# Optimization experiments

Measured on AMD Instinct MI355X. Metric: run time of the kernel, lower is better.

The kernel has to match this reference:

```python
import jax, jax.numpy as jnp
import numpy as np

N_NODES = 100000
N_EDGES = 1600000


def _cheb_norm(edge_index, num_nodes):
    # PyG ChebConv norm with sym normalization, lambda_max=2:
    # remove self-loops, L = I - D^-1/2 A D^-1/2, scale by 2/lambda_max (=1),
    # add self-loops with -1 -> diagonal nets to 0, leaving w = -d^-1/2 d^-1/2 on edges.
    src, dst = edge_index[0], edge_index[1]
    mask = (src != dst).astype(jnp.float32)  # remove_self_loops
    deg = jax.ops.segment_sum(mask, src, num_segments=num_nodes)
    dinv = jnp.where(deg > 0, jax.lax.rsqrt(jnp.maximum(deg, 1.0)), 0.0)
    w = -dinv[src] * dinv[dst] * mask
    return w


def _cheb_conv(x, src, dst, w_edge, W, b, num_nodes):
    # W: [K=3, C_in, C_out], Chebyshev recurrence T0=x, T1=Lx, T2=2L T1 - T0
    def prop(h):
        return jax.ops.segment_sum(w_edge[:, None] * h[src], dst, num_segments=num_nodes)

    tx0 = x
    tx1 = prop(x)
    tx2 = 2.0 * prop(tx1) - tx0
    out = tx0 @ W[0] + tx1 @ W[1] + tx2 @ W[2] + b
    return out


def setup_inputs() -> dict:
    key = jax.random.key(0)
    ks = jax.random.split(key, 10)
    x = jax.random.normal(ks[0], (N_NODES, 128), dtype=jnp.float32)
    edge_index = jax.random.randint(ks[1], (2, N_EDGES), 0, N_NODES, dtype=jnp.int64)
    batch = jnp.zeros((N_NODES,), dtype=jnp.int64)

    def glorot(k, shape):
        fan = shape[-2] + shape[-1]
        return jax.random.uniform(k, shape, jnp.float32, -1.0, 1.0) * np.sqrt(6.0 / fan)

    W1 = glorot(ks[2], (3, 128, 64))
    b1 = jnp.zeros((64,), jnp.float32)
    W2 = glorot(ks[3], (3, 64, 128))
    b2 = jnp.zeros((128,), jnp.float32)
    W3 = glorot(ks[4], (3, 128, 256))
    b3 = jnp.zeros((256,), jnp.float32)
    return {"x": x, "edge_index": edge_index, "batch": batch,
            "W1": W1, "b1": b1, "W2": W2, "b2": b2, "W3": W3, "b3": b3}


def reference(x, edge_index, batch, W1, b1, W2, b2, W3, b3):
    num_nodes = x.shape[0]
    src, dst = edge_index[0], edge_index[1]
    w_edge = _cheb_norm(edge_index, num_nodes)
    h = jax.nn.relu(_cheb_conv(x, src, dst, w_edge, W1, b1, num_nodes))
    h = jax.nn.relu(_cheb_conv(h, src, dst, w_edge, W2, b2, num_nodes))
    h = _cheb_conv(h, src, dst, w_edge, W3, b3, num_nodes)
    return h
```

## Files before the change

kernel.cpp:

```cpp
#include <hip/hip_runtime.h>

#define N_NODES 100000
#define N_EDGES 1600000
#define CAP 64
#define GB 6250
#define GM 782

typedef short short8 __attribute__((ext_vector_type(8)));
typedef float f32x4 __attribute__((ext_vector_type(4)));

__device__ __forceinline__ unsigned short f2b(float f) {
    unsigned u = __builtin_bit_cast(unsigned, f);
    u += 0x7fffu + ((u >> 16) & 1u);
    return (unsigned short)(u >> 16);
}
__device__ __forceinline__ float b2f_lo(unsigned p) {
    return __builtin_bit_cast(float, p << 16);
}
__device__ __forceinline__ float b2f_hi(unsigned p) {
    return __builtin_bit_cast(float, p & 0xffff0000u);
}

__global__ __launch_bounds__(256) void k_fat(const int* __restrict__ src, const int* __restrict__ dst,
                                             float* __restrict__ degout, int* __restrict__ cnt,
                                             int* __restrict__ slots,
                                             const float* __restrict__ x, const float* __restrict__ W1,
                                             const float* __restrict__ b1,
                                             const float* __restrict__ W2, const float* __restrict__ W3,
                                             unsigned short* __restrict__ vub,
                                             unsigned short* __restrict__ Wt2,
                                             unsigned short* __restrict__ Wt3) {
    constexpr int KT = 128, KP = KT + 8, NFR = 4;
    __shared__ unsigned short sw[64 * KP];
    const int tid = threadIdx.x;
    int bid = blockIdx.x;

    if (bid < GB) {
        int e = bid * 256 + tid;
        int s = src[e], d = dst[e];
        if (s != d) {
            atomicAdd(&degout[s], 1.0f);
            int pos = atomicAdd(&cnt[d], 1);
            if (pos < CAP) slots[(size_t)d * CAP + pos] = s;
        }
        return;
    }
    bid -= GB;
    if (bid < 3 * GM) {
        const int sl = bid / GM, mb = bid % GM;
        const int n0 = sl * 64;

        for (int i = tid; i < 64 * 128; i += 256) {
            int k = i >> 6;
            int r = i & 63;
            int co = r + n0;
            float v;
            if (co < 64)       v = W1[(128 + k) * 64 + co];
            else if (co < 128) v = W1[(256 + k) * 64 + (co - 64)];
            else               v = W1[k * 64 + (co - 128)] - W1[(256 + k) * 64 + (co - 128)];
            sw[r * KP + k] = f2b(v);
        }
        __syncthreads();

        const int wave = tid >> 6, lane = tid & 63;
        const int l16 = lane & 15, quad = lane >> 4;
        const int mBase = mb * 128 + wave * 32;
        const int r0 = mBase + l16, r1 = mBase + 16 + l16;
        const bool in0 = r0 < N_NODES, in1 = r1 < N_NODES;

        f32x4 acc[2][NFR] = {};
        const short8 zero8 = {0, 0, 0, 0, 0, 0, 0, 0};

        #pragma unroll
        for (int kt = 0; kt < KT / 32; kt++) {
            const int kin = kt * 32 + quad * 8;
            short8 a0 = zero8, a1 = zero8;
            if (in0) {
                const float* px = x + (size_t)r0 * 128 + kin;
                float4 f0 = *(const float4*)px, f1 = *(const float4*)(px + 4);
                a0[0] = (short)f2b(f0.x); a0[1] = (short)f2b(f0.y);
                a0[2] = (short)f2b(f0.z); a0[3] = (short)f2b(f0.w);
                a0[4] = (short)f2b(f1.x); a0[5] = (short)f2b(f1.y);
                a0[6] = (short)f2b(f1.z); a0[7] = (short)f2b(f1.w);
            }
            if (in1) {
                const float* px = x + (size_t)r1 * 128 + kin;
                float4 f0 = *(const float4*)px, f1 = *(const float4*)(px + 4);
                a1[0] = (short)f2b(f0.x); a1[1] = (short)f2b(f0.y);
                a1[2] = (short)f2b(f0.z); a1[3] = (short)f2b(f0.w);
                a1[4] = (short)f2b(f1.x); a1[5] = (short)f2b(f1.y);
                a1[6] = (short)f2b(f1.z); a1[7] = (short)f2b(f1.w);
            }
            #pragma unroll
            for (int nf = 0; nf < NFR; nf++) {
                const short8 b = *(const short8*)(sw + (nf * 16 + l16) * KP + kt * 32 + quad * 8);
                acc[0][nf] = __builtin_amdgcn_mfma_f32_16x16x32_bf16(a0, b, acc[0][nf], 0, 0, 0);
                acc[1][nf] = __builtin_amdgcn_mfma_f32_16x16x32_bf16(a1, b, acc[1][nf], 0, 0, 0);
            }
        }

        #pragma unroll
        for (int mi = 0; mi < 2; mi++) {
            #pragma unroll
            for (int nf = 0; nf < NFR; nf++) {
                #pragma unroll
                for (int r = 0; r < 4; r++) {
                    const int node = mBase + mi * 16 + quad * 4 + r;
                    if (node < N_NODES) {
                        const int co = n0 + nf * 16 + l16;
                        float o = acc[mi][nf][r] + (co >= 128 ? b1[co - 128] : 0.f);
                        vub[(size_t)node * 192 + co] = f2b(o);
                    }
                }
            }
        }
        return;
    }
    bid -= 3 * GM;
    if (bid < 96) {
        int j = bid * 256 + tid;
        int k = j % 192, n = j / 192;
        Wt2[(size_t)n * 192 + k] = f2b(W2[(size_t)k * 128 + n]);
        return;
    }
    bid -= 96;
    {
        int j = bid * 256 + tid;
        int k = j % 384, n = j / 384;
        Wt3[(size_t)n * 384 + k] = f2b(W3[(size_t)k * 256 + n]);
    }
}

__global__ void k_dinv(float* __restrict__ deg) {
    int n = blockIdx.x * blockDim.x + threadIdx.x;
    if (n < N_NODES) {
        float dg = deg[n];
        deg[n] = dg > 0.f ? rsqrtf(dg) : 0.f;
    }
}

template <int C, bool RELU>
__global__ __launch_bounds__(256) void k_gather7(const unsigned short* __restrict__ h,
                                                 int hStride,
                                                 const int* __restrict__ cnt,
                                                 const int* __restrict__ slots,
                                                 const float* __restrict__ dinv,
                                                 float alpha,
                                                 const unsigned short* __restrict__ init,
                                                 int iStride,
                                                 float beta,
                                                 unsigned short* __restrict__ out) {
    const int wave = threadIdx.x >> 6;
    const int lane = threadIdx.x & 63;
    const int half = lane >> 5;
    const int l32  = lane & 31;
    const int n0 = (blockIdx.x * 4 + wave) * 2;
    if (n0 >= N_NODES) return;
    const int n1 = n0 + 1;
    const int m0 = min(cnt[n0], CAP);
    const int m1 = min(cnt[n1], CAP);
    const int nMy = half ? n1 : n0;

    int c0l = 0, c1l = 0;
    float w0f = 0.f, w1f = 0.f;
    if (lane < m0) { c0l = slots[(size_t)n0 * CAP + lane]; w0f = dinv[c0l]; }
    if (lane < m1) { c1l = slots[(size_t)n1 * CAP + lane]; w1f = dinv[c1l]; }
    const int w0i = __builtin_bit_cast(int, w0f);
    const int w1i = __builtin_bit_cast(int, w1f);

    const int mhi = max(m0, m1);
    const float scale = -alpha * dinv[nMy];

    if (C == 128) {
        const uint2* h4 = (const uint2*)h;
        float ax = 0.f, ay = 0.f, az = 0.f, aw = 0.f;
        for (int j = 0; j < mhi; j += 8) {
            #pragma unroll
            for (int k = 0; k < 8; k++) {
                int cA = __builtin_amdgcn_readlane(c0l, j + k);
                int cB = __builtin_amdgcn_readlane(c1l, j + k);
                float wA = __builtin_bit_cast(float, __builtin_amdgcn_readlane(w0i, j + k));
                float wB = __builtin_bit_cast(float, __builtin_amdgcn_readlane(w1i, j + k));
                int c = half ? cB : cA;
                float w = half ? wB : wA;
                uint2 q = h4[(size_t)c * hStride + l32];
                ax = fmaf(w, b2f_lo(q.x), ax); ay = fmaf(w, b2f_hi(q.x), ay);
                az = fmaf(w, b2f_lo(q.y), az); aw = fmaf(w, b2f_hi(q.y), aw);
            }
        }
        float vx = scale * ax, vy = scale * ay, vz = scale * az, vw = scale * aw;
        if (init) {
            uint2 ip = ((const uint2*)init)[(size_t)nMy * iStride + l32];
            vx = fmaf(beta, b2f_lo(ip.x), vx); vy = fmaf(beta, b2f_hi(ip.x), vy);
            vz = fmaf(beta, b2f_lo(ip.y), vz); vw = fmaf(beta, b2f_hi(ip.y), vw);
        }
        if (RELU) {
            vx = fmaxf(vx, 0.f); vy = fmaxf(vy, 0.f);
            vz = fmaxf(vz, 0.f); vw = fmaxf(vw, 0.f);
        }
        uint2 o;
        o.x = (unsigned)f2b(vx) | ((unsigned)f2b(vy) << 16);
        o.y = (unsigned)f2b(vz) | ((unsigned)f2b(vw) << 16);
        ((uint2*)out)[(size_t)nMy * 32 + l32] = o;
    } else {
        const unsigned* h2 = (const unsigned*)h;
        float ax = 0.f, ay = 0.f;
        for (int j = 0; j < mhi; j += 8) {
            #pragma unroll
            for (int k = 0; k < 8; k++) {
                int cA = __builtin_amdgcn_readlane(c0l, j + k);
                int cB = __builtin_amdgcn_readlane(c1l, j + k);
                float wA = __builtin_bit_cast(float, __builtin_amdgcn_readlane(w0i, j + k));
                float wB = __builtin_bit_cast(float, __builtin_amdgcn_readlane(w1i, j + k));
                int c = half ? cB : cA;
                float w = half ? wB : wA;
                unsigned q = h2[(size_t)c * hStride + l32];
                ax = fmaf(w, b2f_lo(q), ax); ay = fmaf(w, b2f_hi(q), ay);
            }
        }
        float vx = scale * ax, vy = scale * ay;
        if (init) {
            unsigned ip = ((const unsigned*)init)[(size_t)nMy * iStride + l32];
            vx = fmaf(beta, b2f_lo(ip), vx); vy = fmaf(beta, b2f_hi(ip), vy);
        }
        if (RELU) { vx = fmaxf(vx, 0.f); vy = fmaxf(vy, 0.f); }
        ((unsigned*)out)[(size_t)nMy * 32 + l32] =
            (unsigned)f2b(vx) | ((unsigned)f2b(vy) << 16);
    }
}

template <int CIN, int COUT, int NSL, bool RELU, bool BF16OUT>
__global__ __launch_bounds__(256) void k_mm2(const unsigned short* __restrict__ t0,
                                             const unsigned short* __restrict__ t1,
                                             const unsigned short* __restrict__ t2,
                                             const unsigned short* __restrict__ Wt,
                                             const float* __restrict__ bias,
                                             void* __restrict__ outv) {
    constexpr int KT = 3 * CIN;
    constexpr int KP = KT + 8;
    constexpr int NFR = NSL / 16;
    __shared__ unsigned short sw[NSL * KP];

    const int tid = threadIdx.x;
    const int n0 = blockIdx.y * NSL;

    constexpr int CHUNKS = NSL * KT / 8;
    for (int i = tid; i < CHUNKS; i += 256) {
        int row = i / (KT / 8);
        int k8 = i % (KT / 8);
        short8 v = *(const short8*)(Wt + (size_t)(n0 + row) * KT + k8 * 8);
        *(short8*)(sw + row * KP + k8 * 8) = v;
    }
    __syncthreads();

    const int wave = tid >> 6, lane = tid & 63;
    const int l16 = lane & 15, quad = lane >> 4;
    const int mBase = blockIdx.x * 128 + wave * 32;
    const int r0 = mBase + l16, r1 = mBase + 16 + l16;
    const bool in0 = r0 < N_NODES, in1 = r1 < N_NODES;

    f32x4 acc[2][NFR] = {};
    const unsigned short* tb[3] = {t0, t1, t2};
    const short8 zero8 = {0, 0, 0, 0, 0, 0, 0, 0};

    #pragma unroll
    for (int kt = 0; kt < KT / 32; kt++) {
        const int kb = kt * 32;
        const unsigned short* t = tb[kb / CIN];
        const int kin = (kb % CIN) + quad * 8;
        short8 a0 = zero8, a1 = zero8;
        if (in0) a0 = *(const short8*)(t + (size_t)r0 * CIN + kin);
        if (in1) a1 = *(const short8*)(t + (size_t)r1 * CIN + kin);
        #pragma unroll
        for (int nf = 0; nf < NFR; nf++) {
            const short8 b = *(const short8*)(sw + (nf * 16 + l16) * KP + kb + quad * 8);
            acc[0][nf] = __builtin_amdgcn_mfma_f32_16x16x32_bf16(a0, b, acc[0][nf], 0, 0, 0);
            acc[1][nf] = __builtin_amdgcn_mfma_f32_16x16x32_bf16(a1, b, acc[1][nf], 0, 0, 0);
        }
    }

    #pragma unroll
    for (int mi = 0; mi < 2; mi++) {
        #pragma unroll
        for (int nf = 0; nf < NFR; nf++) {
            #pragma unroll
            for (int r = 0; r < 4; r++) {
                const int node = mBase + mi * 16 + quad * 4 + r;
                if (node < N_NODES) {
                    const int co = n0 + nf * 16 + l16;
                    float o = acc[mi][nf][r] + bias[co];
                    if (RELU) o = fmaxf(o, 0.f);
                    if (BF16OUT)
                        ((unsigned short*)outv)[(size_t)node * COUT + co] = f2b(o);
                    else
                        ((float*)outv)[(size_t)node * COUT + co] = o;
                }
            }
        }
    }
}

template <int CIN, int COUT, int NSL>
__global__ __launch_bounds__(256) void k_mm3(const unsigned short* __restrict__ t0,
                                             const unsigned short* __restrict__ t1,
                                             const unsigned short* __restrict__ t2,
                                             const unsigned short* __restrict__ Wt,
                                             const float* __restrict__ bias,
                                             float* __restrict__ out) {
    constexpr int KT = 3 * CIN;
    constexpr int KP = KT + 8;
    constexpr int NFR = NSL / 16;
    constexpr int NSLICES = COUT / NSL;
    constexpr int KSTEPS = KT / 32;
    __shared__ unsigned short sw[NSL * KP];

    const int tid = threadIdx.x;
    const int wave = tid >> 6, lane = tid & 63;
    const int l16 = lane & 15, quad = lane >> 4;
    const int mBase = blockIdx.x * 128 + wave * 32;
    const int r0 = mBase + l16, r1 = mBase + 16 + l16;
    const bool in0 = r0 < N_NODES, in1 = r1 < N_NODES;

    const unsigned short* tb[3] = {t0, t1, t2};
    const short8 zero8 = {0, 0, 0, 0, 0, 0, 0, 0};

    short8 a0[KSTEPS], a1[KSTEPS];
    #pragma unroll
    for (int kt = 0; kt < KSTEPS; kt++) {
        const int kb = kt * 32;
        const unsigned short* t = tb[kb / CIN];
        const int kin = (kb % CIN) + quad * 8;
        a0[kt] = in0 ? *(const short8*)(t + (size_t)r0 * CIN + kin) : zero8;
        a1[kt] = in1 ? *(const short8*)(t + (size_t)r1 * CIN + kin) : zero8;
    }

    constexpr int CHUNKS = NSL * KT / 8;
    for (int ns = 0; ns < NSLICES; ns++) {
        const int n0 = ns * NSL;
        if (ns) __syncthreads();
        for (int i = tid; i < CHUNKS; i += 256) {
            int row = i / (KT / 8);
            int k8 = i % (KT / 8);
            *(short8*)(sw + row * KP + k8 * 8) =
                *(const short8*)(Wt + (size_t)(n0 + row) * KT + k8 * 8);
        }
        __syncthreads();

        f32x4 acc[2][NFR] = {};
        #pragma unroll
        for (int kt = 0; kt < KSTEPS; kt++) {
            #pragma unroll
            for (int nf = 0; nf < NFR; nf++) {
                const short8 b = *(const short8*)(sw + (nf * 16 + l16) * KP + kt * 32 + quad * 8);
                acc[0][nf] = __builtin_amdgcn_mfma_f32_16x16x32_bf16(a0[kt], b, acc[0][nf], 0, 0, 0);
                acc[1][nf] = __builtin_amdgcn_mfma_f32_16x16x32_bf16(a1[kt], b, acc[1][nf], 0, 0, 0);
            }
        }

        #pragma unroll
        for (int mi = 0; mi < 2; mi++) {
            #pragma unroll
            for (int nf = 0; nf < NFR; nf++) {
                #pragma unroll
                for (int r = 0; r < 4; r++) {
                    const int node = mBase + mi * 16 + quad * 4 + r;
                    if (node < N_NODES) {
                        const int co = n0 + nf * 16 + l16;
                        out[(size_t)node * COUT + co] = acc[mi][nf][r] + bias[co];
                    }
                }
            }
        }
    }
}

static inline int ceil_div(int a, int b) { return (a + b - 1) / b; }

extern "C" void kernel_launch(void* const* d_in, const int* in_sizes, int n_in,
                              void* d_out, int out_size, void* d_ws, size_t ws_size,
                              hipStream_t stream) {
    const float* x   = (const float*)d_in[0];
    const int*   ei  = (const int*)d_in[1];
    const int*   src = ei;
    const int*   dst = ei + N_EDGES;
    const float* W1 = (const float*)d_in[3];
    const float* b1 = (const float*)d_in[4];
    const float* W2 = (const float*)d_in[5];
    const float* b2 = (const float*)d_in[6];
    const float* W3 = (const float*)d_in[7];
    const float* b3 = (const float*)d_in[8];
    float* out = (float*)d_out;

    char* p = (char*)d_ws;
    int*   slots  = (int*)p;             p += (size_t)N_NODES * CAP * 4;
    float* dinv   = (float*)p;           p += (size_t)N_NODES * 4;
    int*   cnt    = (int*)p;             p += (size_t)N_NODES * 4;
    unsigned short* tx1b = (unsigned short*)p; p += (size_t)N_NODES * 128 * 2;
    unsigned short* h1b  = (unsigned short*)p; p += (size_t)N_NODES * 64 * 2;
    unsigned short* tx2b = (unsigned short*)p; p += (size_t)N_NODES * 128 * 2;
    unsigned short* h2b  = (unsigned short*)p; p += (size_t)N_NODES * 128 * 2;
    unsigned short* Wt2  = (unsigned short*)p; p += (size_t)128 * 192 * 2;
    unsigned short* Wt3  = (unsigned short*)p; p += (size_t)256 * 384 * 2;
    unsigned short* vub = tx2b;

    const int TB = 256;
    const int gN = ceil_div(N_NODES, TB);
    const int gG = ceil_div(N_NODES, 8);
    const int gM = ceil_div(N_NODES, 128);
    const int FATB = GB + 3 * GM + 96 + 384;

    hipMemsetAsync(dinv, 0, 2 * N_NODES * sizeof(float), stream);
    k_fat<<<FATB, TB, 0, stream>>>(src, dst, dinv, cnt, slots,
                                   x, W1, b1, W2, W3, vub, Wt2, Wt3);
    k_dinv<<<gN, TB, 0, stream>>>(dinv);

    k_gather7<64, false><<<gG, TB, 0, stream>>>(vub + 64, 96, cnt, slots, dinv,
                                                2.f, vub, 96, 1.f, tx1b);
    k_gather7<64, true><<<gG, TB, 0, stream>>>(tx1b, 32, cnt, slots, dinv,
                                               1.f, vub + 128, 96, 1.f, h1b);

    k_gather7<64, false><<<gG, TB, 0, stream>>>(h1b, 32, cnt, slots, dinv,
                                                1.f, nullptr, 0, 0.f, tx1b);
    k_gather7<64, false><<<gG, TB, 0, stream>>>(tx1b, 32, cnt, slots, dinv,
                                                2.f, h1b, 32, -1.f, tx2b);
    k_mm2<64, 128, 128, true, true><<<dim3(gM, 1), TB, 0, stream>>>(h1b, tx1b, tx2b, Wt2, b2, h2b);

    k_gather7<128, false><<<gG, TB, 0, stream>>>(h2b, 32, cnt, slots, dinv,
                                                 1.f, nullptr, 0, 0.f, tx1b);
    k_gather7<128, false><<<gG, TB, 0, stream>>>(tx1b, 32, cnt, slots, dinv,
                                                 2.f, h2b, 32, -1.f, tx2b);
    k_mm3<128, 256, 64><<<dim3(gM, 1), TB, 0, stream>>>(h2b, tx1b, tx2b, Wt3, b3, out);
}
```

Baseline: 770.6 us.

## Reuse loaded x rows across three weight slices and interleave fat-kernel blocks

Each GEMM block in the fused first kernel now loads and converts its 128 rows of x to bf16 once, keeps them in registers, and loops over the three 64-column weight slices itself. Before, three separate blocks each reloaded the same rows. The block index is also permuted with a multiplicative swizzle (7919 mod grid size) so edge-scatter, GEMM and transpose blocks are interleaved across the GPU. This cuts redundant x reads and balances atomic-heavy and MFMA-heavy work. In exchange there are fewer, longer GEMM blocks, extra syncs, more register pressure, and the swizzle is only a bijection if 7919 is coprime with the grid size.

```diff
diff --git a/kernel.cpp b/kernel.cpp
--- a/kernel.cpp
+++ b/kernel.cpp
@@ -5,6 +5,8 @@
 #define CAP 64
 #define GB 6250
 #define GM 782
+#define FATB (GB + GM + 96 + 384)
+#define SWZ 7919
 
 typedef short short8 __attribute__((ext_vector_type(8)));
 typedef float f32x4 __attribute__((ext_vector_type(4)));
@@ -33,7 +35,7 @@
     constexpr int KT = 128, KP = KT + 8, NFR = 4;
     __shared__ unsigned short sw[64 * KP];
     const int tid = threadIdx.x;
-    int bid = blockIdx.x;
+    int bid = (int)(((unsigned)blockIdx.x * SWZ) % FATB);
 
     if (bid < GB) {
         int e = bid * 256 + tid;
@@ -46,77 +48,83 @@
         return;
     }
     bid -= GB;
-    if (bid < 3 * GM) {
-        const int sl = bid / GM, mb = bid % GM;
-        const int n0 = sl * 64;
-
-        for (int i = tid; i < 64 * 128; i += 256) {
-            int k = i >> 6;
-            int r = i & 63;
-            int co = r + n0;
-            float v;
-            if (co < 64)       v = W1[(128 + k) * 64 + co];
-            else if (co < 128) v = W1[(256 + k) * 64 + (co - 64)];
-            else               v = W1[k * 64 + (co - 128)] - W1[(256 + k) * 64 + (co - 128)];
-            sw[r * KP + k] = f2b(v);
-        }
-        __syncthreads();
-
+    if (bid < GM) {
         const int wave = tid >> 6, lane = tid & 63;
         const int l16 = lane & 15, quad = lane >> 4;
-        const int mBase = mb * 128 + wave * 32;
+        const int mBase = bid * 128 + wave * 32;
         const int r0 = mBase + l16, r1 = mBase + 16 + l16;
         const bool in0 = r0 < N_NODES, in1 = r1 < N_NODES;
-
-        f32x4 acc[2][NFR] = {};
         const short8 zero8 = {0, 0, 0, 0, 0, 0, 0, 0};
 
+        short8 a0[4], a1[4];
         #pragma unroll
-        for (int kt = 0; kt < KT / 32; kt++) {
+        for (int kt = 0; kt < 4; kt++) {
             const int kin = kt * 32 + quad * 8;
-            short8 a0 = zero8, a1 = zero8;
+            short8 t0 = zero8, t1 = zero8;
             if (in0) {
                 const float* px = x + (size_t)r0 * 128 + kin;
                 float4 f0 = *(const float4*)px, f1 = *(const float4*)(px + 4);
-                a0[0] = (short)f2b(f0.x); a0[1] = (short)f2b(f0.y);
-                a0[2] = (short)f2b(f0.z); a0[3] = (short)f2b(f0.w);
-                a0[4] = (short)f2b(f1.x); a0[5] = (short)f2b(f1.y);
-                a0[6] = (short)f2b(f1.z); a0[7] = (short)f2b(f1.w);
+                t0[0] = (short)f2b(f0.x); t0[1] = (short)f2b(f0.y);
+                t0[2] = (short)f2b(f0.z); t0[3] = (short)f2b(f0.w);
+                t0[4] = (short)f2b(f1.x); t0[5] = (short)f2b(f1.y);
+                t0[6] = (short)f2b(f1.z); t0[7] = (short)f2b(f1.w);
             }
             if (in1) {
                 const float* px = x + (size_t)r1 * 128 + kin;
                 float4 f0 = *(const float4*)px, f1 = *(const float4*)(px + 4);
-                a1[0] = (short)f2b(f0.x); a1[1] = (short)f2b(f0.y);
-                a1[2] = (short)f2b(f0.z); a1[3] = (short)f2b(f0.w);
-                a1[4] = (short)f2b(f1.x); a1[5] = (short)f2b(f1.y);
-                a1[6] = (short)f2b(f1.z); a1[7] = (short)f2b(f1.w);
-            }
-            #pragma unroll
-            for (int nf = 0; nf < NFR; nf++) {
-                const short8 b = *(const short8*)(sw + (nf * 16 + l16) * KP + kt * 32 + quad * 8);
-                acc[0][nf] = __builtin_amdgcn_mfma_f32_16x16x32_bf16(a0, b, acc[0][nf], 0, 0, 0);
-                acc[1][nf] = __builtin_amdgcn_mfma_f32_16x16x32_bf16(a1, b, acc[1][nf], 0, 0, 0);
-            }
-        }
-
-        #pragma unroll
-        for (int mi = 0; mi < 2; mi++) {
-            #pragma unroll
-            for (int nf = 0; nf < NFR; nf++) {
+                t1[0] = (short)f2b(f0.x); t1[1] = (short)f2b(f0.y);
+                t1[2] = (short)f2b(f0.z); t1[3] = (short)f2b(f0.w);
+                t1[4] = (short)f2b(f1.x); t1[5] = (short)f2b(f1.y);
+                t1[6] = (short)f2b(f1.z); t1[7] = (short)f2b(f1.w);
+            }
+            a0[kt] = t0; a1[kt] = t1;
+        }
+
+        for (int sl = 0; sl < 3; sl++) {
+            const int n0 = sl * 64;
+            if (sl) __syncthreads();
+            for (int i = tid; i < 64 * 128; i += 256) {
+                int k = i >> 6;
+                int r = i & 63;
+                int co = r + n0;
+                float v;
+                if (co < 64)       v = W1[(128 + k) * 64 + co];
+                else if (co < 128) v = W1[(256 + k) * 64 + (co - 64)];
+                else               v = W1[k * 64 + (co - 128)] - W1[(256 + k) * 64 + (co - 128)];
+                sw[r * KP + k] = f2b(v);
+            }
+            __syncthreads();
+
+            f32x4 acc[2][NFR] = {};
+            #pragma unroll
+            for (int kt = 0; kt < 4; kt++) {
                 #pragma unroll
-                for (int r = 0; r < 4; r++) {
-                    const int node = mBase + mi * 16 + quad * 4 + r;
-                    if (node < N_NODES) {
-                        const int co = n0 + nf * 16 + l16;
-                        float o = acc[mi][nf][r] + (co >= 128 ? b1[co - 128] : 0.f);
-                        vub[(size_t)node * 192 + co] = f2b(o);
+                for (int nf = 0; nf < NFR; nf++) {
+                    const short8 b = *(const short8*)(sw + (nf * 16 + l16) * KP + kt * 32 + quad * 8);
+                    acc[0][nf] = __builtin_amdgcn_mfma_f32_16x16x32_bf16(a0[kt], b, acc[0][nf], 0, 0, 0);
+                    acc[1][nf] = __builtin_amdgcn_mfma_f32_16x16x32_bf16(a1[kt], b, acc[1][nf], 0, 0, 0);
+                }
+            }
+
+            #pragma unroll
+            for (int mi = 0; mi < 2; mi++) {
+                #pragma unroll
+                for (int nf = 0; nf < NFR; nf++) {
+                    #pragma unroll
+                    for (int r = 0; r < 4; r++) {
+                        const int node = mBase + mi * 16 + quad * 4 + r;
+                        if (node < N_NODES) {
+                            const int co = n0 + nf * 16 + l16;
+                            float o = acc[mi][nf][r] + (co >= 128 ? b1[co - 128] : 0.f);
+                            vub[(size_t)node * 192 + co] = f2b(o);
+                        }
                     }
                 }
             }
         }
         return;
     }
-    bid -= 3 * GM;
+    bid -= GM;
     if (bid < 96) {
         int j = bid * 256 + tid;
         int k = j % 192, n = j / 192;
@@ -407,7 +415,6 @@
     const int gN = ceil_div(N_NODES, TB);
     const int gG = ceil_div(N_NODES, 8);
     const int gM = ceil_div(N_NODES, 128);
-    const int FATB = GB + 3 * GM + 96 + 384;
 
     hipMemsetAsync(dinv, 0, 2 * N_NODES * sizeof(float), stream);
     k_fat<<<FATB, TB, 0, stream>>>(src, dst, dinv, cnt, slots,
```

Measured after the change: 734.8 us. 4.6% less time.
